# Kernel optimization log

Hardware: AMD Instinct MI355X
Metric: run time of the kernel (lower is better)

Reference implementation:

```python
import jax, jax.numpy as jnp
import numpy as np

D = 2048   # input_size = hidden1 = hidden2 = output_size
MH = 32    # meta_weight hidden size (3 -> MH -> 1 MLP with ReLU)


def setup_inputs() -> dict:
    key = jax.random.key(0)
    ks = jax.random.split(key, 8)
    def lin(k, out_d, in_d):
        return jax.random.normal(k, (out_d, in_d), jnp.float32) / np.float32(np.sqrt(in_d))
    return {
        "x": jax.random.normal(ks[0], (1, D), jnp.float32),
        "W1": lin(ks[1], D, D), "b1": jnp.zeros((D,), jnp.float32),
        "W2": lin(ks[2], D, D), "b2": jnp.zeros((D,), jnp.float32),
        "W3": lin(ks[3], D, D), "b3": jnp.zeros((D,), jnp.float32),
        "Wm1": jax.random.normal(ks[4], (3, MH), jnp.float32) / np.float32(np.sqrt(3.0)),
        "bm1": jnp.zeros((MH,), jnp.float32),
        "Wm2": jax.random.normal(ks[5], (MH, 1), jnp.float32) / np.float32(np.sqrt(MH)),
        "bm2": jnp.zeros((1,), jnp.float32),
    }


def _meta_update(W, inp, outp, Wm1, bm1, Wm2, bm2):
    # W: [O, I] (torch Linear weight layout), inp: [1, I] pre-layer activation,
    # outp: [1, O] post-layer activation. meta_inputs[o, i] = (v_i, w_oi, v_o),
    # matching torch.stack((input_stack, layer, output_stack), dim=2).
    O, I = W.shape
    mi = jnp.stack(
        [jnp.broadcast_to(inp[0][None, :], (O, I)),
         W,
         jnp.broadcast_to(outp[0][:, None], (O, I))],
        axis=-1)                                   # [O, I, 3]
    h = jax.nn.relu(jnp.einsum("oik,km->oim", mi, Wm1) + bm1)  # [O, I, MH]
    new_w = jnp.einsum("oim,mn->oin", h, Wm2)[..., 0] + bm2[0]  # [O, I]
    return new_w


def reference(x, W1, b1, W2, b2, W3, b3, Wm1, bm1, Wm2, bm2):
    # 3-layer MLP forward (ReLU after every layer, including the last)
    a0 = x
    a1 = jax.nn.relu(a0 @ W1.T + b1)
    a2 = jax.nn.relu(a1 @ W2.T + b2)
    out = jax.nn.relu(a2 @ W3.T + b3)
    # Vectorized per-weight meta-network updates (replaces the nested Python
    # double for-loop over hidden1*hidden2 scalar meta_weight.forward calls).
    # Updates read original activations/weights, so they are order-independent.
    nW1 = _meta_update(W1, a0, a1, Wm1, bm1, Wm2, bm2)
    nW2 = _meta_update(W2, a1, a2, Wm1, bm1, Wm2, bm2)
    nW3 = _meta_update(W3, a2, out, Wm1, bm1, Wm2, bm2)
    return out, nW1, nW2, nW3
```

## Files before the change

kernel.cpp:

```cpp
#include <hip/hip_runtime.h>

#define DD 2048
#define MHH 32

typedef _Float16 hf2 __attribute__((ext_vector_type(2)));

__device__ __forceinline__ unsigned pack_pair(float lo, float hi) {
    hf2 v;
    v.x = (_Float16)lo;
    v.y = (_Float16)hi;
    return __builtin_bit_cast(unsigned, v);
}

__device__ __forceinline__ hf2 rfl2(unsigned u) {
    u = __builtin_amdgcn_readfirstlane(u);
    return __builtin_bit_cast(hf2, u);
}

__device__ __forceinline__ hf2 dup16(float x) {
    hf2 v;
    v.x = (_Float16)x;
    v.y = v.x;
    return v;
}

__global__ __launch_bounds__(256) void gemv_relu_prep_k(const float* __restrict__ W,
                                                        const float* __restrict__ x,
                                                        const float* __restrict__ b,
                                                        float* __restrict__ y,
                                                        const float* __restrict__ Wm1,
                                                        const float* __restrict__ bm1,
                                                        const float* __restrict__ Wm2,
                                                        unsigned* __restrict__ cst) {
    if (blockIdx.x == DD / 4) {
        const int mp = threadIdx.x;
        if (mp < MHH / 2) {
            const int m = 2 * mp;
            cst[mp]      = pack_pair(Wm1[m],           Wm1[m + 1]);
            cst[16 + mp] = pack_pair(Wm1[MHH + m],     Wm1[MHH + m + 1]);
            cst[32 + mp] = pack_pair(Wm2[m],           Wm2[m + 1]);
            cst[48 + mp] = pack_pair(Wm1[2 * MHH + m], Wm1[2 * MHH + m + 1]);
            cst[64 + mp] = pack_pair(bm1[m],           bm1[m + 1]);
        }
        return;
    }
    const int wave = threadIdx.x >> 6;
    const int lane = threadIdx.x & 63;
    const int row  = (blockIdx.x << 2) + wave;
    const float* Wr = W + (size_t)row * DD;
    float acc = 0.f;
#pragma unroll
    for (int it = 0; it < 8; ++it) {
        const int col = ((it << 6) + lane) << 2;
        const float4 w4 = *reinterpret_cast<const float4*>(Wr + col);
        const float4 x4 = *reinterpret_cast<const float4*>(x + col);
        acc = fmaf(w4.x, x4.x, acc);
        acc = fmaf(w4.y, x4.y, acc);
        acc = fmaf(w4.z, x4.z, acc);
        acc = fmaf(w4.w, x4.w, acc);
    }
#pragma unroll
    for (int off = 32; off > 0; off >>= 1)
        acc += __shfl_down(acc, off, 64);
    if (lane == 0) {
        const float v = acc + b[row];
        y[row] = fmaxf(v, 0.f);
    }
}

__global__ __launch_bounds__(256) void gemv_relu_k(const float* __restrict__ W,
                                                   const float* __restrict__ x,
                                                   const float* __restrict__ b,
                                                   float* __restrict__ y) {
    const int wave = threadIdx.x >> 6;
    const int lane = threadIdx.x & 63;
    const int row  = (blockIdx.x << 2) + wave;
    const float* Wr = W + (size_t)row * DD;
    float acc = 0.f;
#pragma unroll
    for (int it = 0; it < 8; ++it) {
        const int col = ((it << 6) + lane) << 2;
        const float4 w4 = *reinterpret_cast<const float4*>(Wr + col);
        const float4 x4 = *reinterpret_cast<const float4*>(x + col);
        acc = fmaf(w4.x, x4.x, acc);
        acc = fmaf(w4.y, x4.y, acc);
        acc = fmaf(w4.z, x4.z, acc);
        acc = fmaf(w4.w, x4.w, acc);
    }
#pragma unroll
    for (int off = 32; off > 0; off >>= 1)
        acc += __shfl_down(acc, off, 64);
    if (lane == 0) {
        const float v = acc + b[row];
        y[row] = fmaxf(v, 0.f);
    }
}

__global__ __launch_bounds__(256) void meta_k(const float* __restrict__ W1,
                                              const float* __restrict__ W2,
                                              const float* __restrict__ W3,
                                              const float* __restrict__ a0,
                                              const float* __restrict__ a1,
                                              const float* __restrict__ a2,
                                              const float* __restrict__ a3,
                                              const unsigned* __restrict__ cst,
                                              const float* __restrict__ bm2,
                                              float* __restrict__ nW) {
    const int layer = blockIdx.x >> 11;
    const int row   = blockIdx.x & (DD - 1);

    const float* W   = (layer == 0) ? W1 : (layer == 1) ? W2 : W3;
    const float* inp = (layer == 0) ? a0 : (layer == 1) ? a1 : a2;
    const float* oup = (layer == 0) ? a1 : (layer == 1) ? a2 : a3;

    const float* Wr  = W  + (size_t)row * DD;
    float*       nWr = nW + (size_t)layer * DD * DD + (size_t)row * DD;

    const int col0 = threadIdx.x * 4;
    const int col1 = (DD / 2) + threadIdx.x * 4;
    const float4 w4a = *reinterpret_cast<const float4*>(Wr + col0);
    const float4 u4a = *reinterpret_cast<const float4*>(inp + col0);
    const float4 w4b = *reinterpret_cast<const float4*>(Wr + col1);
    const float4 u4b = *reinterpret_cast<const float4*>(inp + col1);

    const uint4* c16 = (const uint4*)cst;
    hf2 Ap[MHH / 2], Bp[MHH / 2], Vp[MHH / 2], Pp[MHH / 2];
#pragma unroll
    for (int j = 0; j < 4; ++j) {
        const uint4 t = c16[j];
        Ap[4 * j + 0] = rfl2(t.x); Ap[4 * j + 1] = rfl2(t.y);
        Ap[4 * j + 2] = rfl2(t.z); Ap[4 * j + 3] = rfl2(t.w);
    }
#pragma unroll
    for (int j = 0; j < 4; ++j) {
        const uint4 t = c16[4 + j];
        Bp[4 * j + 0] = rfl2(t.x); Bp[4 * j + 1] = rfl2(t.y);
        Bp[4 * j + 2] = rfl2(t.z); Bp[4 * j + 3] = rfl2(t.w);
    }
#pragma unroll
    for (int j = 0; j < 4; ++j) {
        const uint4 t = c16[8 + j];
        Vp[4 * j + 0] = rfl2(t.x); Vp[4 * j + 1] = rfl2(t.y);
        Vp[4 * j + 2] = rfl2(t.z); Vp[4 * j + 3] = rfl2(t.w);
    }
    const float ov = oup[row];
    const hf2 ovd = dup16(ov);
#pragma unroll
    for (int j = 0; j < 4; ++j) {
        const uint4 tc = c16[12 + j];
        const uint4 tb = c16[16 + j];
        const hf2 c0v = rfl2(tc.x), c1v = rfl2(tc.y), c2v = rfl2(tc.z), c3v = rfl2(tc.w);
        hf2 b0v = __builtin_bit_cast(hf2, tb.x);
        hf2 b1v = __builtin_bit_cast(hf2, tb.y);
        hf2 b2v = __builtin_bit_cast(hf2, tb.z);
        hf2 b3v = __builtin_bit_cast(hf2, tb.w);
        Pp[4 * j + 0] = __builtin_elementwise_fma(ovd, c0v, b0v);
        Pp[4 * j + 1] = __builtin_elementwise_fma(ovd, c1v, b1v);
        Pp[4 * j + 2] = __builtin_elementwise_fma(ovd, c2v, b2v);
        Pp[4 * j + 3] = __builtin_elementwise_fma(ovd, c3v, b3v);
        asm volatile("" : "+v"(Pp[4 * j + 0]), "+v"(Pp[4 * j + 1]),
                          "+v"(Pp[4 * j + 2]), "+v"(Pp[4 * j + 3]));
    }
    const float bias2 = bm2[0];

    hf2 u0 = dup16(u4a.x), u1 = dup16(u4a.y), u2 = dup16(u4a.z), u3 = dup16(u4a.w);
    hf2 u4 = dup16(u4b.x), u5 = dup16(u4b.y), u6 = dup16(u4b.z), u7 = dup16(u4b.w);
    hf2 w0 = dup16(w4a.x), w1 = dup16(w4a.y), w2 = dup16(w4a.z), w3 = dup16(w4a.w);
    hf2 w4 = dup16(w4b.x), w5 = dup16(w4b.y), w6 = dup16(w4b.z), w7 = dup16(w4b.w);

    float c0 = 0.f, c1 = 0.f, c2 = 0.f, c3 = 0.f;
    float c4 = 0.f, c5 = 0.f, c6 = 0.f, c7 = 0.f;
    const hf2 zero = (hf2)(_Float16)0.f;

#pragma unroll
    for (int mp = 0; mp < MHH / 2; ++mp) {
        const hf2 a = Ap[mp], b = Bp[mp], v = Vp[mp], p = Pp[mp];
        hf2 q0 = __builtin_elementwise_fma(u0, a, p);
        hf2 q1 = __builtin_elementwise_fma(u1, a, p);
        hf2 q2 = __builtin_elementwise_fma(u2, a, p);
        hf2 q3 = __builtin_elementwise_fma(u3, a, p);
        hf2 q4 = __builtin_elementwise_fma(u4, a, p);
        hf2 q5 = __builtin_elementwise_fma(u5, a, p);
        hf2 q6 = __builtin_elementwise_fma(u6, a, p);
        hf2 q7 = __builtin_elementwise_fma(u7, a, p);
        q0 = __builtin_elementwise_fma(w0, b, q0);
        q1 = __builtin_elementwise_fma(w1, b, q1);
        q2 = __builtin_elementwise_fma(w2, b, q2);
        q3 = __builtin_elementwise_fma(w3, b, q3);
        q4 = __builtin_elementwise_fma(w4, b, q4);
        q5 = __builtin_elementwise_fma(w5, b, q5);
        q6 = __builtin_elementwise_fma(w6, b, q6);
        q7 = __builtin_elementwise_fma(w7, b, q7);
        q0 = __builtin_elementwise_max(q0, zero);
        q1 = __builtin_elementwise_max(q1, zero);
        q2 = __builtin_elementwise_max(q2, zero);
        q3 = __builtin_elementwise_max(q3, zero);
        q4 = __builtin_elementwise_max(q4, zero);
        q5 = __builtin_elementwise_max(q5, zero);
        q6 = __builtin_elementwise_max(q6, zero);
        q7 = __builtin_elementwise_max(q7, zero);
        c0 = __builtin_amdgcn_fdot2(q0, v, c0, false);
        c1 = __builtin_amdgcn_fdot2(q1, v, c1, false);
        c2 = __builtin_amdgcn_fdot2(q2, v, c2, false);
        c3 = __builtin_amdgcn_fdot2(q3, v, c3, false);
        c4 = __builtin_amdgcn_fdot2(q4, v, c4, false);
        c5 = __builtin_amdgcn_fdot2(q5, v, c5, false);
        c6 = __builtin_amdgcn_fdot2(q6, v, c6, false);
        c7 = __builtin_amdgcn_fdot2(q7, v, c7, false);
    }

    float4 r0, r1;
    r0.x = c0 + bias2; r0.y = c1 + bias2; r0.z = c2 + bias2; r0.w = c3 + bias2;
    r1.x = c4 + bias2; r1.y = c5 + bias2; r1.z = c6 + bias2; r1.w = c7 + bias2;
    *reinterpret_cast<float4*>(nWr + col0) = r0;
    *reinterpret_cast<float4*>(nWr + col1) = r1;
}

extern "C" void kernel_launch(void* const* d_in, const int* in_sizes, int n_in,
                              void* d_out, int out_size, void* d_ws, size_t ws_size,
                              hipStream_t stream) {
    const float* x   = (const float*)d_in[0];
    const float* W1  = (const float*)d_in[1];
    const float* b1  = (const float*)d_in[2];
    const float* W2  = (const float*)d_in[3];
    const float* b2  = (const float*)d_in[4];
    const float* W3  = (const float*)d_in[5];
    const float* b3  = (const float*)d_in[6];
    const float* Wm1 = (const float*)d_in[7];
    const float* bm1 = (const float*)d_in[8];
    const float* Wm2 = (const float*)d_in[9];
    const float* bm2 = (const float*)d_in[10];

    float* out = (float*)d_out;
    float* nW  = out + DD;
    float* a1  = (float*)d_ws;
    float* a2  = a1 + DD;
    unsigned* cst = (unsigned*)(a2 + DD);

    gemv_relu_prep_k<<<DD / 4 + 1, 256, 0, stream>>>(W1, x, b1, a1, Wm1, bm1, Wm2, cst);
    gemv_relu_k<<<DD / 4, 256, 0, stream>>>(W2, a1, b2, a2);
    gemv_relu_k<<<DD / 4, 256, 0, stream>>>(W3, a2, b3, out);
    meta_k<<<3 * DD, 256, 0, stream>>>(W1, W2, W3, x, a1, a2, out,
                                       cst, bm2, nW);
}
```

Baseline: 47.45 us.

## Fuse meta updates into later GEMV launches to overlap dependent stages

Splits the meta update into per-layer pieces and runs each one inside the next layer's GEMV kernel: the layer-1 meta update runs alongside the W2 GEMV, layer 2 alongside W3, and layer 3 in a final meta-only kernel. The aim is to fill the mostly idle GPU during the small, latency-bound GEMV launches with useful bandwidth-heavy work, so the serial GEMV chain is no longer pure overhead. The trade-off is that the GEMV blocks now share the kernel with many meta blocks and could be delayed, and the total launch count stays at four.

```diff
diff --git a/kernel.cpp b/kernel.cpp
--- a/kernel.cpp
+++ b/kernel.cpp
@@ -24,29 +24,13 @@
     return v;
 }
 
-__global__ __launch_bounds__(256) void gemv_relu_prep_k(const float* __restrict__ W,
-                                                        const float* __restrict__ x,
-                                                        const float* __restrict__ b,
-                                                        float* __restrict__ y,
-                                                        const float* __restrict__ Wm1,
-                                                        const float* __restrict__ bm1,
-                                                        const float* __restrict__ Wm2,
-                                                        unsigned* __restrict__ cst) {
-    if (blockIdx.x == DD / 4) {
-        const int mp = threadIdx.x;
-        if (mp < MHH / 2) {
-            const int m = 2 * mp;
-            cst[mp]      = pack_pair(Wm1[m],           Wm1[m + 1]);
-            cst[16 + mp] = pack_pair(Wm1[MHH + m],     Wm1[MHH + m + 1]);
-            cst[32 + mp] = pack_pair(Wm2[m],           Wm2[m + 1]);
-            cst[48 + mp] = pack_pair(Wm1[2 * MHH + m], Wm1[2 * MHH + m + 1]);
-            cst[64 + mp] = pack_pair(bm1[m],           bm1[m + 1]);
-        }
-        return;
-    }
+__device__ __forceinline__ void gemv4_body(const float* __restrict__ W,
+                                           const float* __restrict__ x,
+                                           const float* __restrict__ b,
+                                           float* __restrict__ y, int blk) {
     const int wave = threadIdx.x >> 6;
     const int lane = threadIdx.x & 63;
-    const int row  = (blockIdx.x << 2) + wave;
+    const int row  = (blk << 2) + wave;
     const float* Wr = W + (size_t)row * DD;
     float acc = 0.f;
 #pragma unroll
@@ -68,54 +52,12 @@
     }
 }
 
-__global__ __launch_bounds__(256) void gemv_relu_k(const float* __restrict__ W,
-                                                   const float* __restrict__ x,
-                                                   const float* __restrict__ b,
-                                                   float* __restrict__ y) {
-    const int wave = threadIdx.x >> 6;
-    const int lane = threadIdx.x & 63;
-    const int row  = (blockIdx.x << 2) + wave;
-    const float* Wr = W + (size_t)row * DD;
-    float acc = 0.f;
-#pragma unroll
-    for (int it = 0; it < 8; ++it) {
-        const int col = ((it << 6) + lane) << 2;
-        const float4 w4 = *reinterpret_cast<const float4*>(Wr + col);
-        const float4 x4 = *reinterpret_cast<const float4*>(x + col);
-        acc = fmaf(w4.x, x4.x, acc);
-        acc = fmaf(w4.y, x4.y, acc);
-        acc = fmaf(w4.z, x4.z, acc);
-        acc = fmaf(w4.w, x4.w, acc);
-    }
-#pragma unroll
-    for (int off = 32; off > 0; off >>= 1)
-        acc += __shfl_down(acc, off, 64);
-    if (lane == 0) {
-        const float v = acc + b[row];
-        y[row] = fmaxf(v, 0.f);
-    }
-}
-
-__global__ __launch_bounds__(256) void meta_k(const float* __restrict__ W1,
-                                              const float* __restrict__ W2,
-                                              const float* __restrict__ W3,
-                                              const float* __restrict__ a0,
-                                              const float* __restrict__ a1,
-                                              const float* __restrict__ a2,
-                                              const float* __restrict__ a3,
+__device__ __forceinline__ void meta_row_body(const float* __restrict__ Wr,
+                                              const float* __restrict__ inp,
+                                              const float ov,
                                               const unsigned* __restrict__ cst,
-                                              const float* __restrict__ bm2,
-                                              float* __restrict__ nW) {
-    const int layer = blockIdx.x >> 11;
-    const int row   = blockIdx.x & (DD - 1);
-
-    const float* W   = (layer == 0) ? W1 : (layer == 1) ? W2 : W3;
-    const float* inp = (layer == 0) ? a0 : (layer == 1) ? a1 : a2;
-    const float* oup = (layer == 0) ? a1 : (layer == 1) ? a2 : a3;
-
-    const float* Wr  = W  + (size_t)row * DD;
-    float*       nWr = nW + (size_t)layer * DD * DD + (size_t)row * DD;
-
+                                              const float bias2,
+                                              float* __restrict__ nWr) {
     const int col0 = threadIdx.x * 4;
     const int col1 = (DD / 2) + threadIdx.x * 4;
     const float4 w4a = *reinterpret_cast<const float4*>(Wr + col0);
@@ -143,7 +85,6 @@
         Vp[4 * j + 0] = rfl2(t.x); Vp[4 * j + 1] = rfl2(t.y);
         Vp[4 * j + 2] = rfl2(t.z); Vp[4 * j + 3] = rfl2(t.w);
     }
-    const float ov = oup[row];
     const hf2 ovd = dup16(ov);
 #pragma unroll
     for (int j = 0; j < 4; ++j) {
@@ -161,7 +102,6 @@
         asm volatile("" : "+v"(Pp[4 * j + 0]), "+v"(Pp[4 * j + 1]),
                           "+v"(Pp[4 * j + 2]), "+v"(Pp[4 * j + 3]));
     }
-    const float bias2 = bm2[0];
 
     hf2 u0 = dup16(u4a.x), u1 = dup16(u4a.y), u2 = dup16(u4a.z), u3 = dup16(u4a.w);
     hf2 u4 = dup16(u4b.x), u5 = dup16(u4b.y), u6 = dup16(u4b.z), u7 = dup16(u4b.w);
@@ -216,6 +156,59 @@
     *reinterpret_cast<float4*>(nWr + col1) = r1;
 }
 
+__global__ __launch_bounds__(256) void gemv_relu_prep_k(const float* __restrict__ W,
+                                                        const float* __restrict__ x,
+                                                        const float* __restrict__ b,
+                                                        float* __restrict__ y,
+                                                        const float* __restrict__ Wm1,
+                                                        const float* __restrict__ bm1,
+                                                        const float* __restrict__ Wm2,
+                                                        unsigned* __restrict__ cst) {
+    if (blockIdx.x == DD / 4) {
+        const int mp = threadIdx.x;
+        if (mp < MHH / 2) {
+            const int m = 2 * mp;
+            cst[mp]      = pack_pair(Wm1[m],           Wm1[m + 1]);
+            cst[16 + mp] = pack_pair(Wm1[MHH + m],     Wm1[MHH + m + 1]);
+            cst[32 + mp] = pack_pair(Wm2[m],           Wm2[m + 1]);
+            cst[48 + mp] = pack_pair(Wm1[2 * MHH + m], Wm1[2 * MHH + m + 1]);
+            cst[64 + mp] = pack_pair(bm1[m],           bm1[m + 1]);
+        }
+        return;
+    }
+    gemv4_body(W, x, b, y, blockIdx.x);
+}
+
+__global__ __launch_bounds__(256) void combo_k(const float* __restrict__ gW,
+                                               const float* __restrict__ gx,
+                                               const float* __restrict__ gb,
+                                               float* __restrict__ gy,
+                                               const float* __restrict__ mW,
+                                               const float* __restrict__ minp,
+                                               const float* __restrict__ mov,
+                                               const unsigned* __restrict__ cst,
+                                               const float* __restrict__ bm2,
+                                               float* __restrict__ mnW) {
+    if (blockIdx.x < DD / 4) {
+        gemv4_body(gW, gx, gb, gy, blockIdx.x);
+        return;
+    }
+    const int row = blockIdx.x - DD / 4;
+    meta_row_body(mW + (size_t)row * DD, minp, mov[row], cst, bm2[0],
+                  mnW + (size_t)row * DD);
+}
+
+__global__ __launch_bounds__(256) void meta_only_k(const float* __restrict__ mW,
+                                                   const float* __restrict__ minp,
+                                                   const float* __restrict__ mov,
+                                                   const unsigned* __restrict__ cst,
+                                                   const float* __restrict__ bm2,
+                                                   float* __restrict__ mnW) {
+    const int row = blockIdx.x;
+    meta_row_body(mW + (size_t)row * DD, minp, mov[row], cst, bm2[0],
+                  mnW + (size_t)row * DD);
+}
+
 extern "C" void kernel_launch(void* const* d_in, const int* in_sizes, int n_in,
                               void* d_out, int out_size, void* d_ws, size_t ws_size,
                               hipStream_t stream) {
@@ -232,14 +225,17 @@
     const float* bm2 = (const float*)d_in[10];
 
     float* out = (float*)d_out;
-    float* nW  = out + DD;
+    float* nW1 = out + DD;
+    float* nW2 = nW1 + (size_t)DD * DD;
+    float* nW3 = nW2 + (size_t)DD * DD;
     float* a1  = (float*)d_ws;
     float* a2  = a1 + DD;
     unsigned* cst = (unsigned*)(a2 + DD);
 
     gemv_relu_prep_k<<<DD / 4 + 1, 256, 0, stream>>>(W1, x, b1, a1, Wm1, bm1, Wm2, cst);
-    gemv_relu_k<<<DD / 4, 256, 0, stream>>>(W2, a1, b2, a2);
-    gemv_relu_k<<<DD / 4, 256, 0, stream>>>(W3, a2, b3, out);
-    meta_k<<<3 * DD, 256, 0, stream>>>(W1, W2, W3, x, a1, a2, out,
-                                       cst, bm2, nW);
-}
+    combo_k<<<DD / 4 + DD, 256, 0, stream>>>(W2, a1, b2, a2,
+                                             W1, x, a1, cst, bm2, nW1);
+    combo_k<<<DD / 4 + DD, 256, 0, stream>>>(W3, a2, b3, out,
+                                             W2, a1, a2, cst, bm2, nW2);
+    meta_only_k<<<DD, 256, 0, stream>>>(W3, a2, out, cst, bm2, nW3);
+}
```

Measured after the change: 50.54 us. 6.5% more time.
